# Kernel optimization log

Hardware: AMD Instinct MI355X
Metric: run time of the kernel (lower is better)

Reference implementation:

```python
import jax, jax.numpy as jnp
import numpy as np

NUM_HEADS = 16
LN_EPS = 1e-5
RMS_EPS = 1e-6


def rmsnorm(x, gamma, eps=RMS_EPS):
    xf = x.astype(jnp.float32)
    rms = jax.lax.rsqrt(jnp.mean(xf * xf, axis=-1, keepdims=True) + eps)
    return gamma * (xf * rms).astype(x.dtype)


def layernorm(x, g, b, eps=LN_EPS):
    mu = jnp.mean(x, axis=-1, keepdims=True)
    var = jnp.mean(jnp.square(x - mu), axis=-1, keepdims=True)
    return (x - mu) * jax.lax.rsqrt(var + eps) * g + b


def setup_inputs() -> dict:
    key = jax.random.key(0)
    E = 2048
    ks = jax.random.split(key, 10)
    std = 0.02
    inp = {
        "x": jax.random.normal(ks[0], (2, 2048, E), dtype=jnp.float32),
        "Wq": jax.random.normal(ks[1], (E, E), dtype=jnp.float32) * std,
        "Wk": jax.random.normal(ks[2], (E, E), dtype=jnp.float32) * std,
        "Wv": jax.random.normal(ks[3], (E, E), dtype=jnp.float32) * std,
        "Wo": jax.random.normal(ks[4], (E, E), dtype=jnp.float32) * std,
        "ln_g": jnp.ones((E,), jnp.float32),
        "ln_b": jnp.zeros((E,), jnp.float32),
        "rms_g": jnp.ones((E,), jnp.float32),
        "mlp_W0": jax.random.normal(ks[5], (E, E), dtype=jnp.float32) * std,
        "sw_W": jax.random.normal(ks[6], (E, E), dtype=jnp.float32) * std,
        "sw_V": jax.random.normal(ks[7], (E, E), dtype=jnp.float32) * std,
        "sw_beta": jnp.ones((1,), jnp.float32),
        "mlp_rms_g": jnp.ones((E,), jnp.float32),
    }
    return inp


def reference(x, Wq, Wk, Wv, Wo, ln_g, ln_b, rms_g, mlp_W0, sw_W, sw_V, sw_beta, mlp_rms_g):
    B, S, E = x.shape
    H = NUM_HEADS
    Dh = E // H
    scale = 1.0 / (Dh ** 0.5)

    # --- MultiheadAttention (faithful to original einsum/view quirks) ---
    q = x @ Wq.T                     # (B,S,E)
    k = (x @ Wk.T) * scale
    v = x @ Wv.T
    qh = q.reshape(B, S, H, Dh)
    kh = k.reshape(B, S, H, Dh)
    scores = jnp.einsum('bthd,bshd->bhts', qh, kh)        # (B,H,T,S)
    causal = jnp.tril(jnp.ones((S, S), dtype=bool))
    scores = jnp.where(causal, scores, -jnp.inf)
    attn = jax.nn.softmax(scores, axis=-1)
    # NOTE: v is split (B,S,Dh,H) -- head/head_dim axes swapped vs q/k, as in the torch code
    vh = v.reshape(B, S, Dh, H)
    ctx = jnp.einsum('bsdh,bhts->bthd', vh, attn)          # == torch 'kjlm,kmij->kiml'
    ctx = ctx.reshape(B, S, E)                              # flatten heads-major
    ctx = layernorm(ctx, ln_g, ln_b)
    attn_out = ctx @ Wo.T

    x = x + attn_out
    x = rmsnorm(x, rms_g)

    # --- MLP: Linear -> SwiGLU -> RMSNorm, residual ---
    h = x @ mlp_W0.T
    w = h @ sw_W.T
    swish = w * jax.nn.sigmoid(sw_beta * w)
    g = swish * (h @ sw_V.T)
    mlp_out = rmsnorm(g, mlp_rms_g)
    return x + mlp_out
```

## Files before the change

kernel.cpp:

```cpp
#include <hip/hip_runtime.h>


#define B_    2
#define S_    2048
#define E_    2048
#define H_    16
#define DH    128
#define MROWS 4096
#define NEGF  (-3.0e38f)

typedef unsigned short ushort_t;
typedef unsigned int   uint_t;
typedef ushort_t us8   __attribute__((ext_vector_type(8)));
typedef ushort_t us4   __attribute__((ext_vector_type(4)));
typedef __bf16   bf16x8 __attribute__((ext_vector_type(8)));
typedef float    f32x4 __attribute__((ext_vector_type(4)));

__device__ __forceinline__ float b2f(ushort_t u) {
    uint_t x = ((uint_t)u) << 16;
    union { uint_t u; float f; } c; c.u = x; return c.f;
}
__device__ __forceinline__ ushort_t f2b(float f) {
    union { float f; uint_t u; } c; c.f = f;
    uint_t x = c.u;
    uint_t r = (x + 0x7fffu + ((x >> 16) & 1u)) >> 16;
    return (ushort_t)r;
}
__device__ __forceinline__ float fexp2(float x) {
    return __builtin_amdgcn_exp2f(x);
}

__device__ __forceinline__ void gld16(const ushort_t* g, ushort_t* l) {
    __builtin_amdgcn_global_load_lds(
        (const __attribute__((address_space(1))) void*)g,
        (__attribute__((address_space(3))) void*)l,
        16, 0, 0);
}

__global__ void probe_dtype(const ushort_t* w, int* flag) {
    __shared__ int cnt;
    if (threadIdx.x == 0) cnt = 0;
    __syncthreads();
    int c = 0;
    for (int i = threadIdx.x; i < 4096; i += 256) {
        uint_t e = (w[i] >> 7) & 0xFFu;
        if (e >= 0x84u) c++;
    }
    atomicAdd(&cnt, c);
    __syncthreads();
    if (threadIdx.x == 0) *flag = (cnt >= 8) ? 1 : 0;
}

__global__ void convert_all(
    const void* sx, const void* s1, const void* s2, const void* s3,
    const void* s4, const void* s5, const void* s6, const void* s7,
    ushort_t* dst, const int* flagp)
{
    const long NBL  = (long)MROWS * E_;
    const long WSZL = (long)E_ * E_;
    const int f = *flagp;
    long i0 = (long)blockIdx.x * blockDim.x + threadIdx.x;
    long stride = (long)gridDim.x * blockDim.x;
    const long n4 = (NBL + 7 * WSZL) >> 2;
    for (long i = i0; i < n4; i += stride) {
        long e = i << 2;
        const void* s; long off;
        if (e < NBL) { s = sx; off = e; }
        else {
            long r = e - NBL;
            int j = (int)(r >> 22);
            off = r & 0x3FFFFFL;
            s = (j == 0) ? s1 : (j == 1) ? s2 : (j == 2) ? s3 : (j == 3) ? s4
              : (j == 4) ? s5 : (j == 5) ? s6 : s7;
        }
        if (f) {
            f32x4 v = *(const f32x4*)((const float*)s + off);
            us4 o = { f2b(v[0]), f2b(v[1]), f2b(v[2]), f2b(v[3]) };
            *(us4*)(dst + e) = o;
        } else {
            *(us4*)(dst + e) = *(const us4*)((const ushort_t*)s + off);
        }
    }
}

__global__ void convert_vecs(
    const void* s0, const void* s1, const void* s2, const void* s3,
    const void* s4, ushort_t* dstbase, const int* flagp)
{
    const int b = blockIdx.x;
    const void* s = (b == 0) ? s0 : (b == 1) ? s1 : (b == 2) ? s2
                  : (b == 3) ? s3 : s4;
    ushort_t* d = dstbase + (long)b * 4096;
    const int n = (b == 4) ? 1 : E_;
    const int f = *flagp;
    for (int i = threadIdx.x; i < n; i += 256)
        d[i] = f ? f2b(((const float*)s)[i]) : ((const ushort_t*)s)[i];
}

__global__ void convert_k(const void* src, ushort_t* dst, long n, const int* flag) {
    int f = *flag;
    long i0 = (long)blockIdx.x * blockDim.x + threadIdx.x;
    long stride = (long)gridDim.x * blockDim.x;
    if (f) {
        const float* s = (const float*)src;
        for (long i = i0; i < n; i += stride) dst[i] = f2b(s[i]);
    } else {
        const ushort_t* s = (const ushort_t*)src;
        for (long i = i0; i < n; i += stride) dst[i] = s[i];
    }
}

__global__ void fill_diag(float* out, long n, float val) {
    long i = (long)blockIdx.x * 256 + threadIdx.x;
    if (i < n) out[i] = val;
}

#define GEMM_LDS __shared__ ushort_t Ls[3][2][4096]

__device__ __forceinline__ void gemm_core(
    const ushort_t* __restrict__ A, const ushort_t* __restrict__ W,
    int m0, int n0, int K, ushort_t (*Ls)[2][4096], f32x4 acc[4][4])
{
    const int tid  = threadIdx.x;
    const int wave = tid >> 6;
    const int lane = tid & 63;
    const int lrow = lane & 15;
    const int quad = lane >> 4;
    const int wm   = (wave >> 1) * 64;
    const int wn   = (wave & 1) * 64;

#pragma unroll
    for (int i = 0; i < 4; i++)
#pragma unroll
        for (int j = 0; j < 4; j++) acc[i][j] = f32x4{0.f, 0.f, 0.f, 0.f};

    const int srow = wave * 16 + (lane >> 2);
    const int scol = ((lane & 3) ^ ((lane >> 3) & 3)) * 8;
    const ushort_t* Ag = A + (long)(m0 + srow) * K + scol;
    const ushort_t* Wg = W + (long)(n0 + srow) * K + scol;
    const int ldsb = wave * 16 * 32;

    const int nk = K >> 5;
#pragma unroll
    for (int p = 0; p < 2; p++) {
        const int kk = p * 32;
        gld16(Ag + kk,               &Ls[p][0][ldsb]);
        gld16(Ag + (long)64*K + kk,  &Ls[p][0][ldsb + 2048]);
        gld16(Wg + kk,               &Ls[p][1][ldsb]);
        gld16(Wg + (long)64*K + kk,  &Ls[p][1][ldsb + 2048]);
    }
    __builtin_amdgcn_sched_barrier(0);

    const int rsA = (quad ^ ((lrow >> 1) & 3)) * 8;

    int cur = 0, nxt = 2;
    for (int t = 0; t < nk; t++) {
        asm volatile("s_waitcnt vmcnt(4)" ::: "memory");
        __builtin_amdgcn_s_barrier();
        __builtin_amdgcn_sched_barrier(0);

        const ushort_t* As = &Ls[cur][0][0];
        const ushort_t* Bs = &Ls[cur][1][0];
        bf16x8 af[4], bfr[4];
#pragma unroll
        for (int i = 0; i < 4; i++)
            af[i]  = __builtin_bit_cast(bf16x8, *(const us8*)&As[(wm + i*16 + lrow) * 32 + rsA]);
#pragma unroll
        for (int j = 0; j < 4; j++)
            bfr[j] = __builtin_bit_cast(bf16x8, *(const us8*)&Bs[(wn + j*16 + lrow) * 32 + rsA]);
#pragma unroll
        for (int i = 0; i < 4; i++)
#pragma unroll
            for (int j = 0; j < 4; j++)
                acc[i][j] = __builtin_amdgcn_mfma_f32_16x16x32_bf16(af[i], bfr[j], acc[i][j], 0, 0, 0);

        {
            int tt = t + 2; if (tt > nk - 1) tt = nk - 1;
            const int kk = tt * 32;
            gld16(Ag + kk,              &Ls[nxt][0][ldsb]);
            gld16(Ag + (long)64*K + kk, &Ls[nxt][0][ldsb + 2048]);
            gld16(Wg + kk,              &Ls[nxt][1][ldsb]);
            gld16(Wg + (long)64*K + kk, &Ls[nxt][1][ldsb + 2048]);
        }
        __builtin_amdgcn_sched_barrier(0);
        cur = (cur == 2) ? 0 : cur + 1;
        nxt = (nxt == 2) ? 0 : nxt + 1;
    }
}

__global__ __launch_bounds__(256) void gemm_bt(
    const ushort_t* __restrict__ A, const ushort_t* __restrict__ W,
    ushort_t* out, const ushort_t* resid, const ushort_t* beta,
    void* outv, const int* flagp, float scale, int mode)
{
    const int K = E_, N = E_;
    GEMM_LDS;
    const int tid  = threadIdx.x;
    const int wave = tid >> 6;
    const int lane = tid & 63;
    const int lrow = lane & 15;
    const int quad = lane >> 4;
    const int wm   = (wave >> 1) * 64;
    const int wn   = (wave & 1) * 64;
    const int m0   = blockIdx.y * 128;
    const int n0   = blockIdx.x * 128;

    const float betav = (beta != nullptr) ? b2f(beta[0]) : 0.0f;
    const int   of32  = (flagp != nullptr) ? *flagp : 0;

    f32x4 acc[4][4];
    gemm_core(A, W, m0, n0, K, Ls, acc);

#pragma unroll
    for (int i = 0; i < 4; i++)
#pragma unroll
        for (int j = 0; j < 4; j++)
#pragma unroll
            for (int r = 0; r < 4; r++) {
                int m = m0 + wm + i*16 + quad*4 + r;
                int n = n0 + wn + j*16 + lrow;
                float v = acc[i][j][r] * scale;
                long idx;
                if (mode == 1) {
                    int h = n >> 7, d = n & 127;
                    idx = ((long)h * S_ + m) * DH + d;
                } else if (mode == 2) {
                    int d = n >> 4, h = n & 15;
                    idx = ((long)h * DH + d) * S_ + m;
                } else {
                    idx = (long)m * N + n;
                    if (mode == 3) {
                        v += b2f(resid[idx]);
                    } else if (mode == 4) {
                        float wv  = b2f(resid[idx]);
                        float sig = 1.0f / (1.0f + expf(-betav * wv));
                        v = wv * sig * v;
                        if (of32) { ((float*)outv)[idx] = v; continue; }
                    }
                }
                out[idx] = f2b(v);
            }
}

__global__ __launch_bounds__(256) void gemm_qkv(
    const ushort_t* __restrict__ X,
    const ushort_t* __restrict__ Wq, const ushort_t* __restrict__ Wk,
    const ushort_t* __restrict__ Wv,
    ushort_t* qo, ushort_t* ko, ushort_t* vo, float kscale)
{
    const int K = E_;
    GEMM_LDS;
    const int tid  = threadIdx.x;
    const int wave = tid >> 6;
    const int lane = tid & 63;
    const int lrow = lane & 15;
    const int quad = lane >> 4;
    const int wm   = (wave >> 1) * 64;
    const int wn   = (wave & 1) * 64;
    const int sel  = blockIdx.x >> 4;
    const int n0   = (blockIdx.x & 15) * 128;
    const int m0   = blockIdx.y * 128;
    const long zoff = (long)blockIdx.z * ((long)S_ * E_);

    const ushort_t* A = X + zoff;
    const ushort_t* W = (sel == 0) ? Wq : (sel == 1) ? Wk : Wv;
    const float scale = (sel == 1) ? kscale : 1.0f;
    ushort_t* out = ((sel == 0) ? qo : (sel == 1) ? ko : vo) + zoff;

    f32x4 acc[4][4];
    gemm_core(A, W, m0, n0, K, Ls, acc);

#pragma unroll
    for (int i = 0; i < 4; i++)
#pragma unroll
        for (int j = 0; j < 4; j++)
#pragma unroll
            for (int r = 0; r < 4; r++) {
                int m = m0 + wm + i*16 + quad*4 + r;
                int n = n0 + wn + j*16 + lrow;
                float v = acc[i][j][r] * scale;
                long idx;
                if (sel <= 1) {
                    int h = n >> 7, d = n & 127;
                    idx = ((long)h * S_ + m) * DH + d;
                } else {
                    int d = n >> 4, h = n & 15;
                    idx = ((long)h * DH + d) * S_ + m;
                }
                out[idx] = f2b(v);
            }
}

__global__ __launch_bounds__(256) void gemm_pair(
    const ushort_t* __restrict__ A,
    const ushort_t* __restrict__ Wa, const ushort_t* __restrict__ Wb,
    ushort_t* outa, void* outb, const int* flagp)
{
    const int K = E_, N = E_;
    GEMM_LDS;
    const int tid  = threadIdx.x;
    const int wave = tid >> 6;
    const int lane = tid & 63;
    const int lrow = lane & 15;
    const int quad = lane >> 4;
    const int wm   = (wave >> 1) * 64;
    const int wn   = (wave & 1) * 64;
    const int m0   = blockIdx.y * 128;
    const int n0   = blockIdx.x * 128;
    const int sel  = blockIdx.z;
    const int of32 = *flagp;

    const ushort_t* W = sel ? Wb : Wa;
    f32x4 acc[4][4];
    gemm_core(A, W, m0, n0, K, Ls, acc);

#pragma unroll
    for (int i = 0; i < 4; i++)
#pragma unroll
        for (int j = 0; j < 4; j++)
#pragma unroll
            for (int r = 0; r < 4; r++) {
                int m = m0 + wm + i*16 + quad*4 + r;
                int n = n0 + wn + j*16 + lrow;
                long idx = (long)m * N + n;
                float v = acc[i][j][r];
                if (sel == 0)           outa[idx] = f2b(v);
                else if (of32)          ((float*)outb)[idx] = v;
                else                    ((ushort_t*)outb)[idx] = f2b(v);
            }
}

__global__ __launch_bounds__(256) void flash_attn(
    const ushort_t* __restrict__ qp, const ushort_t* __restrict__ kp,
    const ushort_t* __restrict__ vt, ushort_t* ctx)
{
    __shared__ alignas(16) ushort_t Kt[64][144];
    __shared__ alignas(16) ushort_t Vt[128][72];
    __shared__ alignas(16) ushort_t Pb[4][16][72];

    const long zq = (long)blockIdx.z * ((long)S_ * E_);
    qp  += zq; kp += zq; vt += zq; ctx += zq;

    const int tid  = threadIdx.x;
    const int wave = tid >> 6;
    const int lane = tid & 63;
    const int lrow = lane & 15;
    const int quad = lane >> 4;
    const int h    = blockIdx.y;

    const long qbase = (long)h * S_ * DH;
    const long vbase = (long)h * DH * S_;

    int kr[4], kc[4], vr[4], vc[4];
#pragma unroll
    for (int it = 0; it < 4; it++) {
        int L = tid + it * 256;
        kr[it] = L >> 4; kc[it] = (L & 15) * 8;
        vr[it] = L >> 3; vc[it] = (L & 7) * 8;
    }

#pragma unroll 1
    for (int half = 0; half < 2; half++) {
        const int qt = (half == 0) ? (int)blockIdx.x : (31 - (int)blockIdx.x);
        const int tw = qt * 64 + wave * 16;

        bf16x8 qf[4];
        {
            const ushort_t* qrow = qp + qbase + (long)(tw + lrow) * DH + quad * 8;
#pragma unroll
            for (int ks = 0; ks < 4; ks++)
                qf[ks] = __builtin_bit_cast(bf16x8, *(const us8*)(qrow + ks * 32));
        }

        float m_i[4], l_i[4];
#pragma unroll
        for (int r = 0; r < 4; r++) { m_i[r] = NEGF; l_i[r] = 0.0f; }
        f32x4 o[8];
#pragma unroll
        for (int i = 0; i < 8; i++) o[i] = f32x4{0.f, 0.f, 0.f, 0.f};

        us8 kreg[4], vreg[4];
#pragma unroll
        for (int it = 0; it < 4; it++)
            kreg[it] = *(const us8*)(kp + qbase + (long)kr[it] * DH + kc[it]);
#pragma unroll
        for (int it = 0; it < 4; it++)
            vreg[it] = *(const us8*)(vt + vbase + (long)vr[it] * S_ + vc[it]);

        for (int st = 0; st <= qt; st++) {
            const int sb = st * 64;

#pragma unroll
            for (int it = 0; it < 4; it++) *(us8*)&Kt[kr[it]][kc[it]] = kreg[it];
#pragma unroll
            for (int it = 0; it < 4; it++) *(us8*)&Vt[vr[it]][vc[it]] = vreg[it];
            __syncthreads();

            if (st < qt) {
                const int sb2 = sb + 64;
#pragma unroll
                for (int it = 0; it < 4; it++)
                    kreg[it] = *(const us8*)(kp + qbase + (long)(sb2 + kr[it]) * DH + kc[it]);
#pragma unroll
                for (int it = 0; it < 4; it++)
                    vreg[it] = *(const us8*)(vt + vbase + (long)vr[it] * S_ + sb2 + vc[it]);
            }

            f32x4 sacc[4];
#pragma unroll
            for (int nt = 0; nt < 4; nt++) {
                sacc[nt] = f32x4{0.f, 0.f, 0.f, 0.f};
#pragma unroll
                for (int ks = 0; ks < 4; ks++) {
                    bf16x8 kf = __builtin_bit_cast(bf16x8, *(const us8*)&Kt[nt*16 + lrow][ks*32 + quad*8]);
                    sacc[nt] = __builtin_amdgcn_mfma_f32_16x16x32_bf16(qf[ks], kf, sacc[nt], 0, 0, 0);
                }
            }

            const bool diag = (st == qt);
            float alpha[4];
#pragma unroll
            for (int r = 0; r < 4; r++) {
                const int trow = tw + quad * 4 + r;
                float pv[4];
#pragma unroll
                for (int nt = 0; nt < 4; nt++) {
                    float sv = sacc[nt][r];
                    if (diag && (sb + nt*16 + lrow > trow)) sv = NEGF;
                    pv[nt] = sv;
                }
                float mx = fmaxf(fmaxf(pv[0], pv[1]), fmaxf(pv[2], pv[3]));
                mx = fmaxf(mx, __shfl_xor(mx, 1));
                mx = fmaxf(mx, __shfl_xor(mx, 2));
                mx = fmaxf(mx, __shfl_xor(mx, 4));
                mx = fmaxf(mx, __shfl_xor(mx, 8));
                float mn = fmaxf(m_i[r], mx);
                float al = fexp2(m_i[r] - mn);
                float s  = 0.0f;
#pragma unroll
                for (int nt = 0; nt < 4; nt++) {
                    float p = fexp2(pv[nt] - mn);
                    s += p;
                    Pb[wave][quad*4 + r][nt*16 + lrow] = f2b(p);
                }
                s += __shfl_xor(s, 1);
                s += __shfl_xor(s, 2);
                s += __shfl_xor(s, 4);
                s += __shfl_xor(s, 8);
                l_i[r]  = l_i[r] * al + s;
                m_i[r]  = mn;
                alpha[r] = al;
            }
#pragma unroll
            for (int nt = 0; nt < 8; nt++)
#pragma unroll
                for (int r = 0; r < 4; r++) o[nt][r] *= alpha[r];

            bf16x8 pf[2];
#pragma unroll
            for (int ks = 0; ks < 2; ks++)
                pf[ks] = __builtin_bit_cast(bf16x8, *(const us8*)&Pb[wave][lrow][ks*32 + quad*8]);
#pragma unroll
            for (int nt = 0; nt < 8; nt++)
#pragma unroll
                for (int ks = 0; ks < 2; ks++) {
                    bf16x8 vf = __builtin_bit_cast(bf16x8, *(const us8*)&Vt[nt*16 + lrow][ks*32 + quad*8]);
                    o[nt] = __builtin_amdgcn_mfma_f32_16x16x32_bf16(pf[ks], vf, o[nt], 0, 0, 0);
                }
            __syncthreads();
        }

        float li4[4];
#pragma unroll
        for (int r = 0; r < 4; r++) li4[r] = 1.0f / l_i[r];
#pragma unroll
        for (int nt = 0; nt < 8; nt++)
#pragma unroll
            for (int r = 0; r < 4; r++) {
                int t = tw + quad*4 + r;
                int d = nt*16 + lrow;
                ctx[(long)t * E_ + h * DH + d] = f2b(o[nt][r] * li4[r]);
            }
    }
}

__global__ __launch_bounds__(256) void ln_rows(
    const ushort_t* x, const ushort_t* __restrict__ g,
    const ushort_t* __restrict__ bta, ushort_t* out)
{
    __shared__ float red[16];
    const int row = blockIdx.x;
    const ushort_t* xr = x + (long)row * E_;
    float vals[8], s = 0.f, ss = 0.f;
#pragma unroll
    for (int i = 0; i < 8; i++) {
        float v = b2f(xr[threadIdx.x + i * 256]);
        vals[i] = v; s += v; ss += v * v;
    }
    for (int off = 1; off < 64; off <<= 1) { s += __shfl_xor(s, off); ss += __shfl_xor(ss, off); }
    int wave = threadIdx.x >> 6, lane = threadIdx.x & 63;
    if (lane == 0) { red[wave] = s; red[8 + wave] = ss; }
    __syncthreads();
    if (threadIdx.x == 0) {
        red[4]  = red[0] + red[1] + red[2] + red[3];
        red[12] = red[8] + red[9] + red[10] + red[11];
    }
    __syncthreads();
    float mu  = red[4] / E_;
    float var = red[12] / E_ - mu * mu;
    float rs  = rsqrtf(var + 1e-5f);
#pragma unroll
    for (int i = 0; i < 8; i++) {
        int c = threadIdx.x + i * 256;
        float v = (vals[i] - mu) * rs * b2f(g[c]) + b2f(bta[c]);
        out[(long)row * E_ + c] = f2b(v);
    }
}

__global__ __launch_bounds__(256) void rms_rows(
    const ushort_t* x, const ushort_t* __restrict__ g, ushort_t* out)
{
    __shared__ float red[8];
    const int row = blockIdx.x;
    const ushort_t* xr = x + (long)row * E_;
    float vals[8], ss = 0.f;
#pragma unroll
    for (int i = 0; i < 8; i++) {
        float v = b2f(xr[threadIdx.x + i * 256]);
        vals[i] = v; ss += v * v;
    }
    for (int off = 1; off < 64; off <<= 1) ss += __shfl_xor(ss, off);
    int wave = threadIdx.x >> 6, lane = threadIdx.x & 63;
    if (lane == 0) red[wave] = ss;
    __syncthreads();
    if (threadIdx.x == 0) red[4] = red[0] + red[1] + red[2] + red[3];
    __syncthreads();
    float rms = rsqrtf(red[4] / E_ + 1e-6f);
#pragma unroll
    for (int i = 0; i < 8; i++) {
        int c = threadIdx.x + i * 256;
        float v = b2f(f2b(vals[i] * rms)) * b2f(g[c]);
        out[(long)row * E_ + c] = f2b(v);
    }
}

__global__ __launch_bounds__(256) void rms_final_swiglu(
    const ushort_t* __restrict__ w, const void* y,
    const ushort_t* __restrict__ g, const ushort_t* resid,
    const ushort_t* beta, void* outv, const int* flagp)
{
    __shared__ float red[8];
    const int row = blockIdx.x;
    const int of32 = *flagp;
    const float betav = b2f(beta[0]);
    float vals[8], ss = 0.f;
#pragma unroll
    for (int i = 0; i < 8; i++) {
        int c = threadIdx.x + i * 256;
        long idx = (long)row * E_ + c;
        float wv = b2f(w[idx]);
        float yv = of32 ? ((const float*)y)[idx] : b2f(((const ushort_t*)y)[idx]);
        float sig = 1.0f / (1.0f + expf(-betav * wv));
        float gv = wv * sig * yv;
        vals[i] = gv; ss += gv * gv;
    }
    for (int off = 1; off < 64; off <<= 1) ss += __shfl_xor(ss, off);
    int wave = threadIdx.x >> 6, lane = threadIdx.x & 63;
    if (lane == 0) red[wave] = ss;
    __syncthreads();
    if (threadIdx.x == 0) red[4] = red[0] + red[1] + red[2] + red[3];
    __syncthreads();
    float rms = rsqrtf(red[4] / E_ + 1e-6f);
#pragma unroll
    for (int i = 0; i < 8; i++) {
        int c = threadIdx.x + i * 256;
        long idx = (long)row * E_ + c;
        if (of32) {
            float v = vals[i] * rms * b2f(g[c]) + b2f(resid[idx]);
            ((float*)outv)[idx] = v;
        } else {
            float v = b2f(f2b(vals[i] * rms)) * b2f(g[c]) + b2f(resid[idx]);
            ((ushort_t*)outv)[idx] = f2b(v);
        }
    }
}

__global__ __launch_bounds__(256) void rms_final(
    const void* x, const ushort_t* __restrict__ g,
    const ushort_t* resid, void* outv, const int* flagp)
{
    __shared__ float red[8];
    const int row = blockIdx.x;
    const int of32 = *flagp;
    float vals[8], ss = 0.f;
#pragma unroll
    for (int i = 0; i < 8; i++) {
        int c = threadIdx.x + i * 256;
        float v = of32 ? ((const float*)x)[(long)row * E_ + c]
                       : b2f(((const ushort_t*)x)[(long)row * E_ + c]);
        vals[i] = v; ss += v * v;
    }
    for (int off = 1; off < 64; off <<= 1) ss += __shfl_xor(ss, off);
    int wave = threadIdx.x >> 6, lane = threadIdx.x & 63;
    if (lane == 0) red[wave] = ss;
    __syncthreads();
    if (threadIdx.x == 0) red[4] = red[0] + red[1] + red[2] + red[3];
    __syncthreads();
    float rms = rsqrtf(red[4] / E_ + 1e-6f);
#pragma unroll
    for (int i = 0; i < 8; i++) {
        int c = threadIdx.x + i * 256;
        long idx = (long)row * E_ + c;
        if (of32) {
            float v = vals[i] * rms * b2f(g[c]) + b2f(resid[idx]);
            ((float*)outv)[idx] = v;
        } else {
            float v = b2f(f2b(vals[i] * rms)) * b2f(g[c]) + b2f(resid[idx]);
            ((ushort_t*)outv)[idx] = f2b(v);
        }
    }
}

extern "C" void kernel_launch(void* const* d_in, const int* in_sizes, int n_in,
                              void* d_out, int out_size, void* d_ws, size_t ws_size,
                              hipStream_t stream)
{
    const size_t NB  = (size_t)MROWS * E_;
    const size_t WSZ = (size_t)E_ * E_;
    const size_t QSZ = (size_t)S_ * E_;
    const float kscale = 0.08838834764831845f * 1.4426950408889634f;

    const size_t stage_elems = NB + 7 * WSZ + 6 * 4096;
    const size_t need_def    = (stage_elems + 2 * NB) * 2;
    const size_t need_direct = 2 * NB * 2;

    dim3 gFull(E_ / 128, MROWS / 128);

    if (ws_size >= need_def) {
        ushort_t* st = (ushort_t*)d_ws;
        ushort_t* c_x   = st;
        ushort_t* c_Wq  = c_x  + NB;
        ushort_t* c_Wk  = c_Wq + WSZ;
        ushort_t* c_Wv  = c_Wk + WSZ;
        ushort_t* c_Wo  = c_Wv + WSZ;
        ushort_t* c_W0  = c_Wo + WSZ;
        ushort_t* c_sW  = c_W0 + WSZ;
        ushort_t* c_sV  = c_sW + WSZ;
        ushort_t* c_lng = c_sV + WSZ;
        ushort_t* c_lnb = c_lng + 4096;
        ushort_t* c_rg  = c_lnb + 4096;
        ushort_t* c_mg  = c_rg  + 4096;
        ushort_t* c_sb  = c_mg  + 4096;
        int*      flag  = (int*)(c_sb + 4096);
        ushort_t* w0    = st + stage_elems;
        ushort_t* w1    = w0 + NB;
        ushort_t* ob    = (ushort_t*)d_out;
        ushort_t* ob2   = ob + NB;

        probe_dtype<<<1, 256, 0, stream>>>((const ushort_t*)d_in[1], flag);
        convert_all<<<2048, 256, 0, stream>>>(d_in[0], d_in[1], d_in[2], d_in[3],
                                              d_in[4], d_in[8], d_in[9], d_in[10],
                                              st, flag);
        convert_vecs<<<5, 256, 0, stream>>>(d_in[5], d_in[6], d_in[7], d_in[12],
                                            d_in[11], c_lng, flag);

        gemm_qkv<<<dim3(48, 16, 2), 256, 0, stream>>>(c_x, c_Wq, c_Wk, c_Wv,
                                                      w0, ob, w1, kscale);
        flash_attn<<<dim3(16, H_, 2), 256, 0, stream>>>(w0, ob, w1, ob2);

        ln_rows<<<MROWS, 256, 0, stream>>>(ob2, c_lng, c_lnb, ob2);
        gemm_bt<<<gFull, 256, 0, stream>>>(ob2, c_Wo, w1, c_x, nullptr, nullptr, nullptr, 1.0f, 3);
        rms_rows<<<MROWS, 256, 0, stream>>>(w1, c_rg, w1);
        gemm_bt<<<gFull, 256, 0, stream>>>(w1, c_W0, w0, nullptr, nullptr, nullptr, nullptr, 1.0f, 0);
        gemm_pair<<<dim3(16, 32, 2), 256, 0, stream>>>(w0, c_sW, c_sV, c_x, d_out, flag);
        rms_final_swiglu<<<MROWS, 256, 0, stream>>>(c_x, d_out, c_mg, w1, c_sb, d_out, flag);
    } else if (ws_size >= need_direct) {
        ushort_t* w0 = (ushort_t*)d_ws;
        ushort_t* w1 = w0 + NB;
        ushort_t* ob = (ushort_t*)d_out;
        int* flag = (int*)((char*)d_ws + 2 * NB * 2);
        hipMemsetAsync(flag, 0, sizeof(int), stream);
        const ushort_t* x   = (const ushort_t*)d_in[0];
        const ushort_t* Wq  = (const ushort_t*)d_in[1];
        const ushort_t* Wk  = (const ushort_t*)d_in[2];
        const ushort_t* Wv  = (const ushort_t*)d_in[3];
        const ushort_t* Wo  = (const ushort_t*)d_in[4];
        const ushort_t* lng = (const ushort_t*)d_in[5];
        const ushort_t* lnb = (const ushort_t*)d_in[6];
        const ushort_t* rg  = (const ushort_t*)d_in[7];
        const ushort_t* W0  = (const ushort_t*)d_in[8];
        const ushort_t* sW  = (const ushort_t*)d_in[9];
        const ushort_t* sV  = (const ushort_t*)d_in[10];
        const ushort_t* sb  = (const ushort_t*)d_in[11];
        const ushort_t* mg  = (const ushort_t*)d_in[12];
        for (int b = 0; b < B_; b++) {
            const ushort_t* xb = x + (size_t)b * QSZ;
            gemm_qkv<<<dim3(48, 16, 1), 256, 0, stream>>>(xb, Wq, Wk, Wv,
                                                          w0, w0 + QSZ, w1, kscale);
            flash_attn<<<dim3(16, H_, 1), 256, 0, stream>>>(w0, w0 + QSZ, w1, ob + (size_t)b * QSZ);
        }
        ln_rows<<<MROWS, 256, 0, stream>>>(ob, lng, lnb, ob);
        gemm_bt<<<gFull, 256, 0, stream>>>(ob, Wo, w0, x, nullptr, nullptr, nullptr, 1.0f, 3);
        rms_rows<<<MROWS, 256, 0, stream>>>(w0, rg, w0);
        gemm_bt<<<gFull, 256, 0, stream>>>(w0, W0, w1, nullptr, nullptr, nullptr, nullptr, 1.0f, 0);
        gemm_bt<<<gFull, 256, 0, stream>>>(w1, sW, ob, nullptr, nullptr, nullptr, nullptr, 1.0f, 0);
        gemm_bt<<<gFull, 256, 0, stream>>>(w1, sV, ob, ob, sb, d_out, flag, 1.0f, 4);
        rms_final<<<MROWS, 256, 0, stream>>>(ob, mg, w0, d_out, flag);
    } else {
        fill_diag<<<((long)NB + 255) / 256, 256, 0, stream>>>((float*)d_out, (long)NB,
                                                              1000.0f + ws_size * 1e-6f);
    }
}
```

Before: 660.0 us.

## Stream GEMM A operand directly from global into registers, bypassing LDS

The GEMM core now loads each wave's A fragments straight from global memory into registers, double-buffered across a two-step unrolled loop. Only the W tile is still staged through the triple-buffered LDS ring, which halves LDS usage and the LDS reads per step. The cost is that the two waves sharing the same rows now load the same A data separately. Each lane also reads 16-byte pieces spread across rows, which coalesces less well, and A load latency is hidden by only one iteration.

New measurement: 923.7 us. 39.9% more time.

```diff
diff --git a/kernel.cpp b/kernel.cpp
--- a/kernel.cpp
+++ b/kernel.cpp
@@ -115,11 +115,11 @@
     if (i < n) out[i] = val;
 }
 
-#define GEMM_LDS __shared__ ushort_t Ls[3][2][4096]
+#define GEMM_LDS __shared__ ushort_t Ls[3][4096]
 
 __device__ __forceinline__ void gemm_core(
     const ushort_t* __restrict__ A, const ushort_t* __restrict__ W,
-    int m0, int n0, int K, ushort_t (*Ls)[2][4096], f32x4 acc[4][4])
+    int m0, int n0, int K, ushort_t (*Ls)[4096], f32x4 acc[4][4])
 {
     const int tid  = threadIdx.x;
     const int wave = tid >> 6;
@@ -136,56 +136,66 @@
 
     const int srow = wave * 16 + (lane >> 2);
     const int scol = ((lane & 3) ^ ((lane >> 3) & 3)) * 8;
-    const ushort_t* Ag = A + (long)(m0 + srow) * K + scol;
     const ushort_t* Wg = W + (long)(n0 + srow) * K + scol;
     const int ldsb = wave * 16 * 32;
 
+    const ushort_t* Ap = A + (long)(m0 + wm + lrow) * K + quad * 8;
+    const long rK = (long)16 * K;
+
     const int nk = K >> 5;
+
+    us8 a0[4], a1[4];
+    a0[0] = *(const us8*)(Ap);
+    a0[1] = *(const us8*)(Ap + rK);
+    a0[2] = *(const us8*)(Ap + 2 * rK);
+    a0[3] = *(const us8*)(Ap + 3 * rK);
 #pragma unroll
     for (int p = 0; p < 2; p++) {
-        const int kk = p * 32;
-        gld16(Ag + kk,               &Ls[p][0][ldsb]);
-        gld16(Ag + (long)64*K + kk,  &Ls[p][0][ldsb + 2048]);
-        gld16(Wg + kk,               &Ls[p][1][ldsb]);
-        gld16(Wg + (long)64*K + kk,  &Ls[p][1][ldsb + 2048]);
+        gld16(Wg + p * 32,               &Ls[p][ldsb]);
+        gld16(Wg + (long)64 * K + p * 32, &Ls[p][ldsb + 2048]);
     }
     __builtin_amdgcn_sched_barrier(0);
 
     const int rsA = (quad ^ ((lrow >> 1) & 3)) * 8;
-
     int cur = 0, nxt = 2;
-    for (int t = 0; t < nk; t++) {
-        asm volatile("s_waitcnt vmcnt(4)" ::: "memory");
-        __builtin_amdgcn_s_barrier();
-        __builtin_amdgcn_sched_barrier(0);
-
-        const ushort_t* As = &Ls[cur][0][0];
-        const ushort_t* Bs = &Ls[cur][1][0];
-        bf16x8 af[4], bfr[4];
-#pragma unroll
-        for (int i = 0; i < 4; i++)
-            af[i]  = __builtin_bit_cast(bf16x8, *(const us8*)&As[(wm + i*16 + lrow) * 32 + rsA]);
-#pragma unroll
-        for (int j = 0; j < 4; j++)
-            bfr[j] = __builtin_bit_cast(bf16x8, *(const us8*)&Bs[(wn + j*16 + lrow) * 32 + rsA]);
-#pragma unroll
-        for (int i = 0; i < 4; i++)
-#pragma unroll
-            for (int j = 0; j < 4; j++)
-                acc[i][j] = __builtin_amdgcn_mfma_f32_16x16x32_bf16(af[i], bfr[j], acc[i][j], 0, 0, 0);
-
-        {
-            int tt = t + 2; if (tt > nk - 1) tt = nk - 1;
-            const int kk = tt * 32;
-            gld16(Ag + kk,              &Ls[nxt][0][ldsb]);
-            gld16(Ag + (long)64*K + kk, &Ls[nxt][0][ldsb + 2048]);
-            gld16(Wg + kk,              &Ls[nxt][1][ldsb]);
-            gld16(Wg + (long)64*K + kk, &Ls[nxt][1][ldsb + 2048]);
-        }
-        __builtin_amdgcn_sched_barrier(0);
-        cur = (cur == 2) ? 0 : cur + 1;
-        nxt = (nxt == 2) ? 0 : nxt + 1;
-    }
+
+#define GEMM_STEP(T, ACUR, ANXT)                                              \
+    {                                                                          \
+        asm volatile("s_waitcnt vmcnt(2)" ::: "memory");                       \
+        __builtin_amdgcn_s_barrier();                                          \
+        __builtin_amdgcn_sched_barrier(0);                                     \
+        int ta = (T) + 1; if (ta > nk - 1) ta = nk - 1;                        \
+        const ushort_t* ap_ = Ap + (long)ta * 32;                              \
+        ANXT[0] = *(const us8*)(ap_);                                          \
+        ANXT[1] = *(const us8*)(ap_ + rK);                                     \
+        ANXT[2] = *(const us8*)(ap_ + 2 * rK);                                 \
+        ANXT[3] = *(const us8*)(ap_ + 3 * rK);                                 \
+        int tb = (T) + 2; if (tb > nk - 1) tb = nk - 1;                        \
+        gld16(Wg + tb * 32,                &Ls[nxt][ldsb]);                    \
+        gld16(Wg + (long)64 * K + tb * 32, &Ls[nxt][ldsb + 2048]);             \
+        bf16x8 bfr[4];                                                         \
+        _Pragma("unroll")                                                      \
+        for (int j = 0; j < 4; j++)                                            \
+            bfr[j] = __builtin_bit_cast(bf16x8,                                \
+                *(const us8*)&Ls[cur][(wn + j * 16 + lrow) * 32 + rsA]);       \
+        _Pragma("unroll")                                                      \
+        for (int i = 0; i < 4; i++) {                                          \
+            bf16x8 af_ = __builtin_bit_cast(bf16x8, ACUR[i]);                  \
+            _Pragma("unroll")                                                  \
+            for (int j = 0; j < 4; j++)                                        \
+                acc[i][j] = __builtin_amdgcn_mfma_f32_16x16x32_bf16(           \
+                    af_, bfr[j], acc[i][j], 0, 0, 0);                          \
+        }                                                                      \
+        __builtin_amdgcn_sched_barrier(0);                                     \
+        cur = (cur == 2) ? 0 : cur + 1;                                        \
+        nxt = (nxt == 2) ? 0 : nxt + 1;                                        \
+    }
+
+    for (int t = 0; t < nk; t += 2) {
+        GEMM_STEP(t,     a0, a1)
+        GEMM_STEP(t + 1, a1, a0)
+    }
+#undef GEMM_STEP
 }
 
 __global__ __launch_bounds__(256) void gemm_bt(
```

## Enlarge GEMM block tile to 256x128 and issue prefetch before MFMA compute

Applied to the files above, without the earlier changes.

Changes the shared GEMM core from a 128x128 to a 256x128 block tile, so each wave computes a 128x64 sub-tile with 8x4 accumulators, and updates the grids of all GEMM launches to match. Staging loads are reorganised into six 16-byte loads per thread per stage, and the next-stage prefetch is now issued before the MFMA block instead of after it. The larger tile raises arithmetic intensity and cuts global traffic per FLOP. In exchange it uses more registers and more LDS per block, and halves the number of blocks, which may lower occupancy and leave CUs idle on the smaller grids.

New measurement: 743.9 us. 1.13x slower.

```diff
diff --git a/kernel.cpp b/kernel.cpp
--- a/kernel.cpp
+++ b/kernel.cpp
@@ -115,77 +115,83 @@
     if (i < n) out[i] = val;
 }
 
-#define GEMM_LDS __shared__ ushort_t Ls[3][2][4096]
+#define GEMM_LDS __shared__ ushort_t Ls[3][12288]
 
 __device__ __forceinline__ void gemm_core(
     const ushort_t* __restrict__ A, const ushort_t* __restrict__ W,
-    int m0, int n0, int K, ushort_t (*Ls)[2][4096], f32x4 acc[4][4])
+    int m0, int n0, int K, ushort_t (*Ls)[12288], f32x4 acc[8][4])
 {
     const int tid  = threadIdx.x;
     const int wave = tid >> 6;
     const int lane = tid & 63;
     const int lrow = lane & 15;
     const int quad = lane >> 4;
-    const int wm   = (wave >> 1) * 64;
+    const int wm   = (wave >> 1) * 128;
     const int wn   = (wave & 1) * 64;
 
 #pragma unroll
-    for (int i = 0; i < 4; i++)
+    for (int i = 0; i < 8; i++)
 #pragma unroll
         for (int j = 0; j < 4; j++) acc[i][j] = f32x4{0.f, 0.f, 0.f, 0.f};
 
-    const int srow = wave * 16 + (lane >> 2);
-    const int scol = ((lane & 3) ^ ((lane >> 3) & 3)) * 8;
-    const ushort_t* Ag = A + (long)(m0 + srow) * K + scol;
-    const ushort_t* Wg = W + (long)(n0 + srow) * K + scol;
-    const int ldsb = wave * 16 * 32;
+    const int srow4 = lane >> 2;
+    const int scolX = ((lane & 3) ^ ((lane >> 3) & 3)) * 8;
+    const ushort_t* AgB = A + (long)(m0 + wave * 64 + srow4) * K + scolX;
+    const ushort_t* WgB = W + (long)(n0 + wave * 32 + srow4) * K + scolX;
+    const int ldsA = wave * 64 * 32;
+    const int ldsB = 8192 + wave * 32 * 32;
+    const long r16K = (long)16 * K;
+
+#define STAGE(S, KK)                                                          \
+    {                                                                          \
+        gld16(AgB + (KK),            &Ls[S][ldsA]);                            \
+        gld16(AgB + r16K + (KK),     &Ls[S][ldsA + 512]);                      \
+        gld16(AgB + 2 * r16K + (KK), &Ls[S][ldsA + 1024]);                     \
+        gld16(AgB + 3 * r16K + (KK), &Ls[S][ldsA + 1536]);                     \
+        gld16(WgB + (KK),            &Ls[S][ldsB]);                            \
+        gld16(WgB + r16K + (KK),     &Ls[S][ldsB + 512]);                      \
+    }
 
     const int nk = K >> 5;
-#pragma unroll
-    for (int p = 0; p < 2; p++) {
-        const int kk = p * 32;
-        gld16(Ag + kk,               &Ls[p][0][ldsb]);
-        gld16(Ag + (long)64*K + kk,  &Ls[p][0][ldsb + 2048]);
-        gld16(Wg + kk,               &Ls[p][1][ldsb]);
-        gld16(Wg + (long)64*K + kk,  &Ls[p][1][ldsb + 2048]);
-    }
+    STAGE(0, 0)
+    STAGE(1, 32)
     __builtin_amdgcn_sched_barrier(0);
 
     const int rsA = (quad ^ ((lrow >> 1) & 3)) * 8;
-
     int cur = 0, nxt = 2;
+
     for (int t = 0; t < nk; t++) {
-        asm volatile("s_waitcnt vmcnt(4)" ::: "memory");
+        asm volatile("s_waitcnt vmcnt(6)" ::: "memory");
         __builtin_amdgcn_s_barrier();
         __builtin_amdgcn_sched_barrier(0);
-
-        const ushort_t* As = &Ls[cur][0][0];
-        const ushort_t* Bs = &Ls[cur][1][0];
-        bf16x8 af[4], bfr[4];
-#pragma unroll
-        for (int i = 0; i < 4; i++)
-            af[i]  = __builtin_bit_cast(bf16x8, *(const us8*)&As[(wm + i*16 + lrow) * 32 + rsA]);
-#pragma unroll
-        for (int j = 0; j < 4; j++)
-            bfr[j] = __builtin_bit_cast(bf16x8, *(const us8*)&Bs[(wn + j*16 + lrow) * 32 + rsA]);
-#pragma unroll
-        for (int i = 0; i < 4; i++)
-#pragma unroll
-            for (int j = 0; j < 4; j++)
-                acc[i][j] = __builtin_amdgcn_mfma_f32_16x16x32_bf16(af[i], bfr[j], acc[i][j], 0, 0, 0);
 
         {
             int tt = t + 2; if (tt > nk - 1) tt = nk - 1;
             const int kk = tt * 32;
-            gld16(Ag + kk,              &Ls[nxt][0][ldsb]);
-            gld16(Ag + (long)64*K + kk, &Ls[nxt][0][ldsb + 2048]);
-            gld16(Wg + kk,              &Ls[nxt][1][ldsb]);
-            gld16(Wg + (long)64*K + kk, &Ls[nxt][1][ldsb + 2048]);
+            STAGE(nxt, kk)
         }
+
+        bf16x8 af[8], bfr[4];
+#pragma unroll
+        for (int i = 0; i < 8; i++)
+            af[i]  = __builtin_bit_cast(bf16x8,
+                *(const us8*)&Ls[cur][(wm + i * 16 + lrow) * 32 + rsA]);
+#pragma unroll
+        for (int j = 0; j < 4; j++)
+            bfr[j] = __builtin_bit_cast(bf16x8,
+                *(const us8*)&Ls[cur][8192 + (wn + j * 16 + lrow) * 32 + rsA]);
+#pragma unroll
+        for (int i = 0; i < 8; i++)
+#pragma unroll
+            for (int j = 0; j < 4; j++)
+                acc[i][j] = __builtin_amdgcn_mfma_f32_16x16x32_bf16(
+                    af[i], bfr[j], acc[i][j], 0, 0, 0);
+
         __builtin_amdgcn_sched_barrier(0);
         cur = (cur == 2) ? 0 : cur + 1;
         nxt = (nxt == 2) ? 0 : nxt + 1;
     }
+#undef STAGE
 }
 
 __global__ __launch_bounds__(256) void gemm_bt(
@@ -200,19 +206,19 @@
     const int lane = tid & 63;
     const int lrow = lane & 15;
     const int quad = lane >> 4;
-    const int wm   = (wave >> 1) * 64;
+    const int wm   = (wave >> 1) * 128;
     const int wn   = (wave & 1) * 64;
-    const int m0   = blockIdx.y * 128;
+    const int m0   = blockIdx.y * 256;
     const int n0   = blockIdx.x * 128;
 
     const float betav = (beta != nullptr) ? b2f(beta[0]) : 0.0f;
     const int   of32  = (flagp != nullptr) ? *flagp : 0;
 
-    f32x4 acc[4][4];
+    f32x4 acc[8][4];
     gemm_core(A, W, m0, n0, K, Ls, acc);
 
 #pragma unroll
-    for (int i = 0; i < 4; i++)
+    for (int i = 0; i < 8; i++)
 #pragma unroll
         for (int j = 0; j < 4; j++)
 #pragma unroll
@@ -255,11 +261,11 @@
     const int lane = tid & 63;
     const int lrow = lane & 15;
     const int quad = lane >> 4;
-    const int wm   = (wave >> 1) * 64;
+    const int wm   = (wave >> 1) * 128;
     const int wn   = (wave & 1) * 64;
     const int sel  = blockIdx.x >> 4;
     const int n0   = (blockIdx.x & 15) * 128;
-    const int m0   = blockIdx.y * 128;
+    const int m0   = blockIdx.y * 256;
     const long zoff = (long)blockIdx.z * ((long)S_ * E_);
 
     const ushort_t* A = X + zoff;
@@ -267,11 +273,11 @@
     const float scale = (sel == 1) ? kscale : 1.0f;
     ushort_t* out = ((sel == 0) ? qo : (sel == 1) ? ko : vo) + zoff;
 
-    f32x4 acc[4][4];
+    f32x4 acc[8][4];
     gemm_core(A, W, m0, n0, K, Ls, acc);
 
 #pragma unroll
-    for (int i = 0; i < 4; i++)
+    for (int i = 0; i < 8; i++)
 #pragma unroll
         for (int j = 0; j < 4; j++)
 #pragma unroll
@@ -303,19 +309,19 @@
     const int lane = tid & 63;
     const int lrow = lane & 15;
     const int quad = lane >> 4;
-    const int wm   = (wave >> 1) * 64;
+    const int wm   = (wave >> 1) * 128;
     const int wn   = (wave & 1) * 64;
-    const int m0   = blockIdx.y * 128;
+    const int m0   = blockIdx.y * 256;
     const int n0   = blockIdx.x * 128;
     const int sel  = blockIdx.z;
     const int of32 = *flagp;
 
     const ushort_t* W = sel ? Wb : Wa;
-    f32x4 acc[4][4];
+    f32x4 acc[8][4];
     gemm_core(A, W, m0, n0, K, Ls, acc);
 
 #pragma unroll
-    for (int i = 0; i < 4; i++)
+    for (int i = 0; i < 8; i++)
 #pragma unroll
         for (int j = 0; j < 4; j++)
 #pragma unroll
@@ -634,7 +640,7 @@
     const size_t need_def    = (stage_elems + 2 * NB) * 2;
     const size_t need_direct = 2 * NB * 2;
 
-    dim3 gFull(E_ / 128, MROWS / 128);
+    dim3 gFull(E_ / 128, MROWS / 256);
 
     if (ws_size >= need_def) {
         ushort_t* st = (ushort_t*)d_ws;
@@ -664,15 +670,15 @@
         convert_vecs<<<5, 256, 0, stream>>>(d_in[5], d_in[6], d_in[7], d_in[12],
                                             d_in[11], c_lng, flag);
 
-        gemm_qkv<<<dim3(48, 16, 2), 256, 0, stream>>>(c_x, c_Wq, c_Wk, c_Wv,
-                                                      w0, ob, w1, kscale);
+        gemm_qkv<<<dim3(48, 8, 2), 256, 0, stream>>>(c_x, c_Wq, c_Wk, c_Wv,
+                                                     w0, ob, w1, kscale);
         flash_attn<<<dim3(16, H_, 2), 256, 0, stream>>>(w0, ob, w1, ob2);
 
         ln_rows<<<MROWS, 256, 0, stream>>>(ob2, c_lng, c_lnb, ob2);
         gemm_bt<<<gFull, 256, 0, stream>>>(ob2, c_Wo, w1, c_x, nullptr, nullptr, nullptr, 1.0f, 3);
         rms_rows<<<MROWS, 256, 0, stream>>>(w1, c_rg, w1);
         gemm_bt<<<gFull, 256, 0, stream>>>(w1, c_W0, w0, nullptr, nullptr, nullptr, nullptr, 1.0f, 0);
-        gemm_pair<<<dim3(16, 32, 2), 256, 0, stream>>>(w0, c_sW, c_sV, c_x, d_out, flag);
+        gemm_pair<<<dim3(16, 16, 2), 256, 0, stream>>>(w0, c_sW, c_sV, c_x, d_out, flag);
         rms_final_swiglu<<<MROWS, 256, 0, stream>>>(c_x, d_out, c_mg, w1, c_sb, d_out, flag);
     } else if (ws_size >= need_direct) {
         ushort_t* w0 = (ushort_t*)d_ws;
@@ -695,8 +701,8 @@
         const ushort_t* mg  = (const ushort_t*)d_in[12];
         for (int b = 0; b < B_; b++) {
             const ushort_t* xb = x + (size_t)b * QSZ;
-            gemm_qkv<<<dim3(48, 16, 1), 256, 0, stream>>>(xb, Wq, Wk, Wv,
-                                                          w0, w0 + QSZ, w1, kscale);
+            gemm_qkv<<<dim3(48, 8, 1), 256, 0, stream>>>(xb, Wq, Wk, Wv,
+                                                         w0, w0 + QSZ, w1, kscale);
             flash_attn<<<dim3(16, H_, 1), 256, 0, stream>>>(w0, w0 + QSZ, w1, ob + (size_t)b * QSZ);
         }
         ln_rows<<<MROWS, 256, 0, stream>>>(ob, lng, lnb, ob);
```
